# Kernel tuning notes

Hardware: AMD Instinct MI355X
Metric: run time of the kernel (lower is better)

Reference implementation:

```python
import jax, jax.numpy as jnp
import numpy as np

N, E, L, H, C = 50000, 800000, 3, 4, 16
D = H * C  # 64
G = 512    # number of graphs
GRAPH_DIM = 128


def setup_inputs() -> dict:
    key = jax.random.key(0)
    ks = jax.random.split(key, 24)
    s = 0.05
    inp = {
        "x": jax.random.normal(ks[0], (N, D), jnp.float32),
        "edge_attr": jax.random.normal(ks[1], (E, 1), jnp.float32),
        "edge_index": jax.random.randint(ks[2], (2, E), 0, N, jnp.int32),
        "batch": jnp.sort(jax.random.randint(ks[3], (N,), 0, G, jnp.int32)),
        # stacked per-layer TransformerConv params (all layers have in=D)
        "Wq": s * jax.random.normal(ks[4], (L, D, D), jnp.float32),
        "bq": jnp.zeros((L, D), jnp.float32),
        "Wk": s * jax.random.normal(ks[5], (L, D, D), jnp.float32),
        "bk": jnp.zeros((L, D), jnp.float32),
        "Wv": s * jax.random.normal(ks[6], (L, D, D), jnp.float32),
        "bv": jnp.zeros((L, D), jnp.float32),
        "We": s * jax.random.normal(ks[7], (L, 1, D), jnp.float32),  # lin_edge, no bias
        "Wskip": s * jax.random.normal(ks[8], (L, D, D), jnp.float32),
        "bskip": jnp.zeros((L, D), jnp.float32),
        # graph encoder MLP head
        "W1": s * jax.random.normal(ks[9], (D, D), jnp.float32),
        "b1": jnp.zeros((D,), jnp.float32),
        "W2": s * jax.random.normal(ks[10], (D, C), jnp.float32),  # hidden_node_dim=16
        "b2": jnp.zeros((C,), jnp.float32),
        "W3": s * jax.random.normal(ks[11], (C, GRAPH_DIM), jnp.float32),
        "b3": jnp.zeros((GRAPH_DIM,), jnp.float32),
    }
    return inp


def transformer_conv(x, edge_attr, src, dst, Wq, bq, Wk, bk, Wv, bv, We, Wskip, bskip):
    # PyG TransformerConv: concat=True, beta=False, root_weight=True
    q = (x @ Wq + bq).reshape(N, H, C)
    k = (x @ Wk + bk).reshape(N, H, C)
    v = (x @ Wv + bv).reshape(N, H, C)
    e = (edge_attr @ We).reshape(E, H, C)  # lin_edge (no bias)
    kj = k[src] + e                         # [E,H,C]
    qi = q[dst]
    score = jnp.sum(qi * kj, axis=-1) / jnp.sqrt(jnp.float32(C))  # [E,H]
    # scatter softmax over edges sharing the same target node
    smax = jax.ops.segment_max(score, dst, num_segments=N)        # [N,H]
    ex = jnp.exp(score - smax[dst])
    denom = jax.ops.segment_sum(ex, dst, num_segments=N)
    alpha = ex / (denom[dst] + 1e-16)                             # [E,H]
    msg = alpha[..., None] * (v[src] + e)                         # [E,H,C]
    out = jax.ops.segment_sum(msg, dst, num_segments=N).reshape(N, D)
    return out + x @ Wskip + bskip


def reference(x, edge_attr, Wq, bq, Wk, bk, Wv, bv, We, Wskip, bskip,
              W1, b1, W2, b2, W3, b3, edge_index, batch):
    src, dst = edge_index[0], edge_index[1]
    h = x
    for l in range(L):
        h = transformer_conv(h, edge_attr, src, dst, Wq[l], bq[l], Wk[l], bk[l],
                             Wv[l], bv[l], We[l], Wskip[l], bskip[l])
        if l < L - 1:
            h = jax.nn.relu(h)
    node_embeddings = h
    # global mean pool
    sums = jax.ops.segment_sum(h, batch, num_segments=G)
    cnt = jax.ops.segment_sum(jnp.ones((N,), h.dtype), batch, num_segments=G)
    g = sums / jnp.maximum(cnt, 1.0)[:, None]
    # graph encoder MLP
    g = jax.nn.relu(g @ W1 + b1)
    g = jax.nn.relu(g @ W2 + b2)
    graph_features = g @ W3 + b3
    return node_embeddings, graph_features
```

## Files before the change

### kernel.cpp

```cpp
#include <hip/hip_runtime.h>
#include <hip/hip_fp16.h>

#define NN 50000
#define EE 800000
#define LL 3
#define HH 4
#define CC 16
#define DD 64
#define GG 512
#define GRAPH_DIM 128

__global__ void zero_i32(int* p, int n) {
    int i = blockIdx.x * blockDim.x + threadIdx.x;
    if (i < n) p[i] = 0;
}
__global__ void zero_f32(float* p, int n) {
    int i = blockIdx.x * blockDim.x + threadIdx.x;
    if (i < n) p[i] = 0.f;
}

__global__ void hist_kernel(const int* __restrict__ dst, int* __restrict__ counts) {
    int e = blockIdx.x * blockDim.x + threadIdx.x;
    if (e < EE) atomicAdd(&counts[dst[e]], 1);
}

__global__ __launch_bounds__(1024) void scan_kernel(const int* __restrict__ counts,
                                                    int* __restrict__ row_ptr,
                                                    int* __restrict__ writepos) {
    __shared__ int wsum[16];
    int t = threadIdx.x, lane = t & 63, wid = t >> 6;
    int base = 0;
    for (int start = 0; start < NN; start += 1024) {
        int idx = start + t;
        int val = (idx < NN) ? counts[idx] : 0;
        int x = val;
        #pragma unroll
        for (int o = 1; o < 64; o <<= 1) {
            int y = __shfl_up(x, o);
            if (lane >= o) x += y;
        }
        if (lane == 63) wsum[wid] = x;
        __syncthreads();
        if (wid == 0) {
            int s = (lane < 16) ? wsum[lane] : 0;
            #pragma unroll
            for (int o = 1; o < 16; o <<= 1) {
                int y = __shfl_up(s, o);
                if (lane >= o) s += y;
            }
            if (lane < 16) wsum[lane] = s;
        }
        __syncthreads();
        int excl = x - val + base + (wid > 0 ? wsum[wid - 1] : 0);
        if (idx < NN) { row_ptr[idx] = excl; writepos[idx] = excl; }
        int total = wsum[15];
        __syncthreads();
        base += total;
    }
    if (t == 0) row_ptr[NN] = base;
}

__global__ void scatter_kernel(const int* __restrict__ ei, const float* __restrict__ attr,
                               int* __restrict__ writepos,
                               int* __restrict__ src_s, float* __restrict__ attr_s) {
    int e = blockIdx.x * blockDim.x + threadIdx.x;
    if (e < EE) {
        int s = ei[e];
        int d = ei[EE + e];
        int p = atomicAdd(&writepos[d], 1);
        src_s[p] = s;
        attr_s[p] = attr[e];
    }
}

__global__ __launch_bounds__(256) void node_gemm(
    const float* __restrict__ hx,
    const float* __restrict__ Wq, const float* __restrict__ bq,
    const float* __restrict__ Wk, const float* __restrict__ bk,
    const float* __restrict__ Wv, const float* __restrict__ bv,
    const float* __restrict__ Ws, const float* __restrict__ bs,
    float* __restrict__ q, __half* __restrict__ kvh, float* __restrict__ sk)
{
    __shared__ float xs[32 * 64];
    int t = threadIdx.x;
    int node0 = blockIdx.x * 32;

    const float4* src4 = (const float4*)(hx + (size_t)node0 * 64);
    float4* dst4 = (float4*)xs;
    #pragma unroll
    for (int r = 0; r < 2; ++r) {
        int i4 = t + r * 256;
        int node = node0 + (i4 >> 4);
        float4 val = make_float4(0.f, 0.f, 0.f, 0.f);
        if (node < NN) val = src4[i4];
        dst4[i4] = val;
    }
    __syncthreads();

    int mat = t >> 6, j = t & 63;
    const float* W = (mat == 0) ? Wq : (mat == 1) ? Wk : (mat == 2) ? Wv : Ws;
    const float* B = (mat == 0) ? bq : (mat == 1) ? bk : (mat == 2) ? bv : bs;

    float wcol[64];
    #pragma unroll
    for (int i = 0; i < 64; ++i) wcol[i] = W[i * 64 + j];
    float bj = B[j];

    for (int n = 0; n < 32; ++n) {
        int node = node0 + n;
        if (node >= NN) break;
        float acc = bj;
        const float4* xr = (const float4*)(xs + n * 64);
        #pragma unroll
        for (int i4 = 0; i4 < 16; ++i4) {
            float4 xv = xr[i4];
            acc = fmaf(xv.x, wcol[4 * i4 + 0], acc);
            acc = fmaf(xv.y, wcol[4 * i4 + 1], acc);
            acc = fmaf(xv.z, wcol[4 * i4 + 2], acc);
            acc = fmaf(xv.w, wcol[4 * i4 + 3], acc);
        }
        size_t idx = (size_t)node * 64 + j;
        if (mat == 0)      q[idx]  = acc;
        else if (mat == 3) sk[idx] = acc;
        else kvh[idx * 2 + (mat == 2)] = __float2half_rn(acc);
    }
}

static __device__ __forceinline__ float2 h2f2(unsigned u) {
    __half2 h = __builtin_bit_cast(__half2, u);
    return __half22float2(h);
}

static __device__ __forceinline__ int cidx(int e, int p0, int p1) {
    int hi = max(p1 - 1, p0);
    int i = min(e, hi);
    return min(i, EE - 1);
}

static __device__ __forceinline__ void chunk16(
    uint4 u0, uint4 u1, uint4 u2, uint4 u3,
    float4 q0, float4 q1, float4 q2, float4 q3,
    float a, float qw, int e, int p1,
    float* accv, float& den, float& saw)
{
    float vt[16];
    float sc = 0.f;
    float2 f;
    f = h2f2(u0.x); sc = fmaf(q0.x, f.x, sc); vt[0]  = f.y;
    f = h2f2(u0.y); sc = fmaf(q0.y, f.x, sc); vt[1]  = f.y;
    f = h2f2(u0.z); sc = fmaf(q0.z, f.x, sc); vt[2]  = f.y;
    f = h2f2(u0.w); sc = fmaf(q0.w, f.x, sc); vt[3]  = f.y;
    f = h2f2(u1.x); sc = fmaf(q1.x, f.x, sc); vt[4]  = f.y;
    f = h2f2(u1.y); sc = fmaf(q1.y, f.x, sc); vt[5]  = f.y;
    f = h2f2(u1.z); sc = fmaf(q1.z, f.x, sc); vt[6]  = f.y;
    f = h2f2(u1.w); sc = fmaf(q1.w, f.x, sc); vt[7]  = f.y;
    f = h2f2(u2.x); sc = fmaf(q2.x, f.x, sc); vt[8]  = f.y;
    f = h2f2(u2.y); sc = fmaf(q2.y, f.x, sc); vt[9]  = f.y;
    f = h2f2(u2.z); sc = fmaf(q2.z, f.x, sc); vt[10] = f.y;
    f = h2f2(u2.w); sc = fmaf(q2.w, f.x, sc); vt[11] = f.y;
    f = h2f2(u3.x); sc = fmaf(q3.x, f.x, sc); vt[12] = f.y;
    f = h2f2(u3.y); sc = fmaf(q3.y, f.x, sc); vt[13] = f.y;
    f = h2f2(u3.z); sc = fmaf(q3.z, f.x, sc); vt[14] = f.y;
    f = h2f2(u3.w); sc = fmaf(q3.w, f.x, sc); vt[15] = f.y;

    float w = __expf(fmaf(a, qw, sc) * 0.25f);
    if (e >= p1) w = 0.f;
    den += w;
    saw = fmaf(w, a, saw);
    #pragma unroll
    for (int j = 0; j < 16; ++j) accv[j] = fmaf(w, vt[j], accv[j]);
}

#define ATTN_BLOCKS 2048

__global__ __launch_bounds__(256) void node_attn(
    const float* __restrict__ q, const __half* __restrict__ kvh,
    const float* __restrict__ sk, const float* __restrict__ We,
    const int* __restrict__ row_ptr, const int* __restrict__ src_s,
    const float* __restrict__ attr_s,
    float* __restrict__ out, int do_relu, int do_pool,
    const int* __restrict__ batch,
    float* __restrict__ gsum, float* __restrict__ gcnt)
{
    __shared__ float lds[4 * 16 * 68];
    int wid   = threadIdx.x >> 6;
    int lane  = threadIdx.x & 63;
    int eslot = lane & 15;
    int head  = lane >> 4;

    const int NW = ATTN_BLOCKS * 4;
    int node = blockIdx.x * 4 + wid;
    if (node >= NN) return;

    float* buf = lds + wid * (16 * 68);

    const float4* w4 = (const float4*)(We + head * 16);
    float4 w0 = w4[0], w1 = w4[1], w2 = w4[2], w3 = w4[3];
    float wec = We[lane];
    const __half* kvbase = kvh + head * 32;

    int p0c = row_ptr[node], p1c = row_ptr[node + 1];
    int i0 = cidx(p0c + eslot, p0c, p1c);
    int i1 = cidx(p0c + 16 + eslot, p0c, p1c);
    int   s0c = src_s[i0]; float a0c = attr_s[i0];
    int   s1c = src_s[i1]; float a1c = attr_s[i1];

    int nn1 = node + NW;
    int nn1c = (nn1 < NN) ? nn1 : node;
    int p0n = row_ptr[nn1c], p1n = row_ptr[nn1c + 1];

    const float4* qp = (const float4*)(q + (size_t)node * 64 + head * 16);
    float4 qc0 = qp[0], qc1 = qp[1], qc2 = qp[2], qc3 = qp[3];
    float skc = sk[(size_t)node * 64 + lane];

    for (;;) {
        int nx1 = node + NW;
        int nx2 = node + 2 * NW;
        int nx1c = (nx1 < NN) ? nx1 : node;
        int nx2c = (nx2 < NN) ? nx2 : node;

        int p0n2 = row_ptr[nx2c];
        int p1n2 = row_ptr[nx2c + 1];

        int j0 = cidx(p0n + eslot, p0n, p1n);
        int j1 = cidx(p0n + 16 + eslot, p0n, p1n);
        int   s0n = src_s[j0]; float a0n = attr_s[j0];
        int   s1n = src_s[j1]; float a1n = attr_s[j1];

        const float4* qpn = (const float4*)(q + (size_t)nx1c * 64 + head * 16);
        float4 qn0 = qpn[0], qn1 = qpn[1], qn2 = qpn[2], qn3 = qpn[3];
        float skn = sk[(size_t)nx1c * 64 + lane];

        const uint4* kva = (const uint4*)(kvbase + (size_t)s0c * 128);
        uint4 u0 = kva[0], u1 = kva[1], u2 = kva[2], u3 = kva[3];
        const uint4* kvb = (const uint4*)(kvbase + (size_t)s1c * 128);
        uint4 x0 = kvb[0], x1 = kvb[1], x2 = kvb[2], x3 = kvb[3];

        float qw = qc0.x * w0.x;
        qw = fmaf(qc0.y, w0.y, qw); qw = fmaf(qc0.z, w0.z, qw); qw = fmaf(qc0.w, w0.w, qw);
        qw = fmaf(qc1.x, w1.x, qw); qw = fmaf(qc1.y, w1.y, qw); qw = fmaf(qc1.z, w1.z, qw); qw = fmaf(qc1.w, w1.w, qw);
        qw = fmaf(qc2.x, w2.x, qw); qw = fmaf(qc2.y, w2.y, qw); qw = fmaf(qc2.z, w2.z, qw); qw = fmaf(qc2.w, w2.w, qw);
        qw = fmaf(qc3.x, w3.x, qw); qw = fmaf(qc3.y, w3.y, qw); qw = fmaf(qc3.z, w3.z, qw); qw = fmaf(qc3.w, w3.w, qw);

        float accv[16];
        #pragma unroll
        for (int j = 0; j < 16; ++j) accv[j] = 0.f;
        float den = 0.f, saw = 0.f;

        chunk16(u0, u1, u2, u3, qc0, qc1, qc2, qc3,
                a0c, qw, p0c + eslot, p1c, accv, den, saw);
        chunk16(x0, x1, x2, x3, qc0, qc1, qc2, qc3,
                a1c, qw, p0c + 16 + eslot, p1c, accv, den, saw);

        #pragma unroll 1
        for (int p = p0c + 32; p < p1c; p += 16) {
            int e = p + eslot;
            int i = cidx(e, p0c, p1c);
            int s = src_s[i];
            float a = attr_s[i];
            const uint4* kr = (const uint4*)(kvbase + (size_t)s * 128);
            uint4 r0 = kr[0], r1 = kr[1], r2 = kr[2], r3 = kr[3];
            chunk16(r0, r1, r2, r3, qc0, qc1, qc2, qc3,
                    a, qw, e, p1c, accv, den, saw);
        }

        den += __shfl_xor(den, 1); den += __shfl_xor(den, 2);
        den += __shfl_xor(den, 4); den += __shfl_xor(den, 8);
        saw += __shfl_xor(saw, 1); saw += __shfl_xor(saw, 2);
        saw += __shfl_xor(saw, 4); saw += __shfl_xor(saw, 8);

        float4* bw = (float4*)(buf + eslot * 68 + head * 16);
        bw[0] = make_float4(accv[0],  accv[1],  accv[2],  accv[3]);
        bw[1] = make_float4(accv[4],  accv[5],  accv[6],  accv[7]);
        bw[2] = make_float4(accv[8],  accv[9],  accv[10], accv[11]);
        bw[3] = make_float4(accv[12], accv[13], accv[14], accv[15]);
        float tot = 0.f;
        #pragma unroll
        for (int e2 = 0; e2 < 16; ++e2) tot += buf[e2 * 68 + lane];

        float o = fmaf(saw, wec, tot) / (den + 1e-16f) + skc;
        if (do_relu) o = fmaxf(o, 0.f);
        out[(size_t)node * 64 + lane] = o;

        if (do_pool) {
            int b = batch[node];
            atomicAdd(&gsum[(size_t)b * 64 + lane], o);
            if (lane == 0) atomicAdd(&gcnt[b], 1.f);
        }

        node = nx1;
        if (node >= NN) break;
        p0c = p0n; p1c = p1n;
        p0n = p0n2; p1n = p1n2;
        s0c = s0n; a0c = a0n;
        s1c = s1n; a1c = a1n;
        qc0 = qn0; qc1 = qn1; qc2 = qn2; qc3 = qn3;
        skc = skn;
    }
}

__global__ __launch_bounds__(128) void pool_mlp(
    const float* __restrict__ gsum, const float* __restrict__ gcnt,
    const float* __restrict__ W1, const float* __restrict__ b1,
    const float* __restrict__ W2, const float* __restrict__ b2,
    const float* __restrict__ W3, const float* __restrict__ b3,
    float* __restrict__ out)
{
    __shared__ float g[64];
    __shared__ float h1s[64];
    __shared__ float h2s[16];
    int b = blockIdx.x, t = threadIdx.x;

    if (t < 64) {
        float c = gcnt[b];
        g[t] = gsum[(size_t)b * 64 + t] / fmaxf(c, 1.f);
    }
    __syncthreads();
    if (t < 64) {
        float a = b1[t];
        #pragma unroll
        for (int i = 0; i < 64; ++i) a = fmaf(g[i], W1[i * 64 + t], a);
        h1s[t] = fmaxf(a, 0.f);
    }
    __syncthreads();
    if (t < 16) {
        float a = b2[t];
        #pragma unroll
        for (int i = 0; i < 64; ++i) a = fmaf(h1s[i], W2[i * 16 + t], a);
        h2s[t] = fmaxf(a, 0.f);
    }
    __syncthreads();
    float a = b3[t];
    #pragma unroll
    for (int i = 0; i < 16; ++i) a = fmaf(h2s[i], W3[i * 128 + t], a);
    out[(size_t)b * 128 + t] = a;
}

extern "C" void kernel_launch(void* const* d_in, const int* in_sizes, int n_in,
                              void* d_out, int out_size, void* d_ws, size_t ws_size,
                              hipStream_t stream) {
    const float* x         = (const float*)d_in[0];
    const float* edge_attr = (const float*)d_in[1];
    const int*   edge_index= (const int*)d_in[2];
    const int*   batch     = (const int*)d_in[3];
    const float* Wq   = (const float*)d_in[4];
    const float* bq   = (const float*)d_in[5];
    const float* Wk   = (const float*)d_in[6];
    const float* bk   = (const float*)d_in[7];
    const float* Wv   = (const float*)d_in[8];
    const float* bv   = (const float*)d_in[9];
    const float* We   = (const float*)d_in[10];
    const float* Wsk  = (const float*)d_in[11];
    const float* bsk  = (const float*)d_in[12];
    const float* W1   = (const float*)d_in[13];
    const float* b1   = (const float*)d_in[14];
    const float* W2   = (const float*)d_in[15];
    const float* b2   = (const float*)d_in[16];
    const float* W3   = (const float*)d_in[17];
    const float* b3   = (const float*)d_in[18];

    float* out        = (float*)d_out;
    float* node_emb   = out;
    float* graph_feat = out + (size_t)NN * 64;

    float* wsf    = (float*)d_ws;
    float* q      = wsf;
    float* kvf    = q    + (size_t)NN * 64;
    float* skp    = kvf  + (size_t)NN * 64;
    float* h      = skp  + (size_t)NN * 64;
    float* attr_s = h    + (size_t)NN * 64;
    int*   src_s  = (int*)(attr_s + EE);
    int*   row_ptr= src_s + EE;
    int*   wpos   = row_ptr + (NN + 1);
    float* gsum   = (float*)(wpos + NN);
    float* gcnt   = gsum + (size_t)GG * 64;
    __half* kvh   = (__half*)kvf;

    zero_i32<<<(NN + 255) / 256, 256, 0, stream>>>(wpos, NN);
    zero_f32<<<(GG * 64 + GG + 255) / 256, 256, 0, stream>>>(gsum, GG * 64 + GG);
    hist_kernel<<<(EE + 255) / 256, 256, 0, stream>>>(edge_index + EE, wpos);
    scan_kernel<<<1, 1024, 0, stream>>>(wpos, row_ptr, wpos);
    scatter_kernel<<<(EE + 255) / 256, 256, 0, stream>>>(edge_index, edge_attr,
                                                         wpos, src_s, attr_s);

    int gemm_grid = (NN + 31) / 32;

    const float* layer_in = x;
    for (int l = 0; l < LL; ++l) {
        const float* Wq_l = Wq + (size_t)l * 64 * 64;
        const float* Wk_l = Wk + (size_t)l * 64 * 64;
        const float* Wv_l = Wv + (size_t)l * 64 * 64;
        const float* Ws_l = Wsk + (size_t)l * 64 * 64;
        const float* bq_l = bq + (size_t)l * 64;
        const float* bk_l = bk + (size_t)l * 64;
        const float* bv_l = bv + (size_t)l * 64;
        const float* bs_l = bsk + (size_t)l * 64;
        const float* We_l = We + (size_t)l * 64;

        node_gemm<<<gemm_grid, 256, 0, stream>>>(layer_in,
            Wq_l, bq_l, Wk_l, bk_l, Wv_l, bv_l, Ws_l, bs_l,
            q, kvh, skp);

        int last = (l == LL - 1);
        float* dst_h = last ? node_emb : h;
        node_attn<<<ATTN_BLOCKS, 256, 0, stream>>>(q, kvh, skp, We_l,
            row_ptr, src_s, attr_s,
            dst_h, !last, last,
            batch, gsum, gcnt);

        layer_in = h;
    }

    pool_mlp<<<GG, 128, 0, stream>>>(gsum, gcnt, W1, b1, W2, b2, W3, b3, graph_feat);
}
```

Before: 539.2 us.

## Deepen software prefetch pipeline in attention kernel and coalesce fp16 KV stores

The node GEMM now stages K and V results in shared memory and writes interleaved half2 K/V pairs as coalesced 32-bit stores, replacing the strided 16-bit writes. The persistent attention loop extends its prefetch distance: it loads row pointers three nodes ahead, edge indices two nodes ahead, and the first K/V chunk of the next node one iteration early. The We weights are reloaded inside the loop, which lowers register pressure across iterations. The deeper pipeline holds more live registers and could reduce occupancy, and the GEMM needs extra shared memory plus a barrier.

```diff
diff --git a/kernel.cpp b/kernel.cpp
--- a/kernel.cpp
+++ b/kernel.cpp
@@ -82,6 +82,8 @@
     float* __restrict__ q, __half* __restrict__ kvh, float* __restrict__ sk)
 {
     __shared__ float xs[32 * 64];
+    __shared__ float kb[32 * 64];
+    __shared__ float vb[32 * 64];
     int t = threadIdx.x;
     int node0 = blockIdx.x * 32;
 
@@ -122,7 +124,22 @@
         size_t idx = (size_t)node * 64 + j;
         if (mat == 0)      q[idx]  = acc;
         else if (mat == 3) sk[idx] = acc;
-        else kvh[idx * 2 + (mat == 2)] = __float2half_rn(acc);
+        else if (mat == 1) kb[n * 64 + j] = acc;
+        else               vb[n * 64 + j] = acc;
+    }
+    __syncthreads();
+
+    unsigned* kvd = (unsigned*)kvh;
+    #pragma unroll
+    for (int r = 0; r < 8; ++r) {
+        int idx = t + r * 256;
+        int n = idx >> 6, j2 = idx & 63;
+        int nd = node0 + n;
+        if (nd < NN) {
+            __half2 hv = __halves2half2(__float2half_rn(kb[idx]),
+                                        __float2half_rn(vb[idx]));
+            kvd[(size_t)nd * 64 + j2] = __builtin_bit_cast(unsigned, hv);
+        }
     }
 }
 
@@ -193,48 +210,51 @@
     if (node >= NN) return;
 
     float* buf = lds + wid * (16 * 68);
-
-    const float4* w4 = (const float4*)(We + head * 16);
-    float4 w0 = w4[0], w1 = w4[1], w2 = w4[2], w3 = w4[3];
-    float wec = We[lane];
     const __half* kvbase = kvh + head * 32;
-
+    const float4* wep = (const float4*)(We + head * 16);
+
+    int n1 = node + NW;     int n1c = (n1 < NN) ? n1 : node;
+    int n2 = node + 2 * NW; int n2c = (n2 < NN) ? n2 : node;
     int p0c = row_ptr[node], p1c = row_ptr[node + 1];
+    int p0n = row_ptr[n1c],  p1n = row_ptr[n1c + 1];
+    int p0n2 = row_ptr[n2c], p1n2 = row_ptr[n2c + 1];
+
     int i0 = cidx(p0c + eslot, p0c, p1c);
     int i1 = cidx(p0c + 16 + eslot, p0c, p1c);
     int   s0c = src_s[i0]; float a0c = attr_s[i0];
     int   s1c = src_s[i1]; float a1c = attr_s[i1];
-
-    int nn1 = node + NW;
-    int nn1c = (nn1 < NN) ? nn1 : node;
-    int p0n = row_ptr[nn1c], p1n = row_ptr[nn1c + 1];
+    int j0 = cidx(p0n + eslot, p0n, p1n);
+    int j1 = cidx(p0n + 16 + eslot, p0n, p1n);
+    int   s0n = src_s[j0]; float a0n = attr_s[j0];
+    int   s1n = src_s[j1]; float a1n = attr_s[j1];
 
     const float4* qp = (const float4*)(q + (size_t)node * 64 + head * 16);
     float4 qc0 = qp[0], qc1 = qp[1], qc2 = qp[2], qc3 = qp[3];
     float skc = sk[(size_t)node * 64 + lane];
 
+    const uint4* kvp0 = (const uint4*)(kvbase + (size_t)s0c * 128);
+    uint4 u0 = kvp0[0], u1 = kvp0[1], u2 = kvp0[2], u3 = kvp0[3];
+
     for (;;) {
         int nx1 = node + NW;
-        int nx2 = node + 2 * NW;
+        int nx3 = node + 3 * NW;
         int nx1c = (nx1 < NN) ? nx1 : node;
-        int nx2c = (nx2 < NN) ? nx2 : node;
-
-        int p0n2 = row_ptr[nx2c];
-        int p1n2 = row_ptr[nx2c + 1];
-
-        int j0 = cidx(p0n + eslot, p0n, p1n);
-        int j1 = cidx(p0n + 16 + eslot, p0n, p1n);
-        int   s0n = src_s[j0]; float a0n = attr_s[j0];
-        int   s1n = src_s[j1]; float a1n = attr_s[j1];
-
+        int nx3c = (nx3 < NN) ? nx3 : node;
+
+        const uint4* kvb = (const uint4*)(kvbase + (size_t)s1c * 128);
+        uint4 x0 = kvb[0], x1 = kvb[1], x2 = kvb[2], x3 = kvb[3];
+        const uint4* kvn = (const uint4*)(kvbase + (size_t)s0n * 128);
+        uint4 un0 = kvn[0], un1 = kvn[1], un2 = kvn[2], un3 = kvn[3];
+        int p0n3 = row_ptr[nx3c], p1n3 = row_ptr[nx3c + 1];
+        int k0 = cidx(p0n2 + eslot, p0n2, p1n2);
+        int k1 = cidx(p0n2 + 16 + eslot, p0n2, p1n2);
+        int   s0n2 = src_s[k0]; float a0n2 = attr_s[k0];
+        int   s1n2 = src_s[k1]; float a1n2 = attr_s[k1];
         const float4* qpn = (const float4*)(q + (size_t)nx1c * 64 + head * 16);
         float4 qn0 = qpn[0], qn1 = qpn[1], qn2 = qpn[2], qn3 = qpn[3];
         float skn = sk[(size_t)nx1c * 64 + lane];
-
-        const uint4* kva = (const uint4*)(kvbase + (size_t)s0c * 128);
-        uint4 u0 = kva[0], u1 = kva[1], u2 = kva[2], u3 = kva[3];
-        const uint4* kvb = (const uint4*)(kvbase + (size_t)s1c * 128);
-        uint4 x0 = kvb[0], x1 = kvb[1], x2 = kvb[2], x3 = kvb[3];
+        float4 w0 = wep[0], w1 = wep[1], w2 = wep[2], w3 = wep[3];
+        float wec = We[lane];
 
         float qw = qc0.x * w0.x;
         qw = fmaf(qc0.y, w0.y, qw); qw = fmaf(qc0.z, w0.z, qw); qw = fmaf(qc0.w, w0.w, qw);
@@ -290,12 +310,14 @@
 
         node = nx1;
         if (node >= NN) break;
-        p0c = p0n; p1c = p1n;
+        p0c = p0n;  p1c = p1n;
         p0n = p0n2; p1n = p1n2;
-        s0c = s0n; a0c = a0n;
-        s1c = s1n; a1c = a1n;
+        p0n2 = p0n3; p1n2 = p1n3;
+        s0c = s0n;  a0c = a0n;  s1c = s1n;  a1c = a1n;
+        s0n = s0n2; a0n = a0n2; s1n = s1n2; a1n = a1n2;
         qc0 = qn0; qc1 = qn1; qc2 = qn2; qc3 = qn3;
         skc = skn;
+        u0 = un0; u1 = un1; u2 = un2; u3 = un3;
     }
 }
 
```

New measurement: 552.2 us. 2.4% more time.
